# Optimization experiments

Measured on AMD Instinct MI355X. Metric: run time of the kernel, lower is better.

Reference implementation:

```python
import jax, jax.numpy as jnp
import numpy as np

# ---- constant lookup tables (mirror SoftALU registered buffers) ----
def _build_tables():
    n = np.arange(16)
    A, Bq, C = np.meshgrid(n, n, np.arange(2), indexing='ij')
    total = A + Bq + C
    eye16 = np.eye(16, dtype=np.float32)
    eye2 = np.eye(2, dtype=np.float32)
    add_t = eye16[total % 16]        # (16,16,2,16)
    carry_t = eye2[total // 16]      # (16,16,2,2)
    and_t = eye16[n[:, None] & n[None, :]]
    or_t = eye16[n[:, None] | n[None, :]]
    xor_t = eye16[n[:, None] ^ n[None, :]]
    bb = np.arange(256)
    b2n = np.zeros((256, 32), np.float32)
    b2n[bb, bb >> 4] = 1.0
    b2n[bb, 16 + (bb & 15)] = 1.0
    return tuple(jnp.asarray(t) for t in (add_t, carry_t, and_t, or_t, xor_t, b2n, b2n.T))

ADD_T, CARRY_T, AND_T, OR_T, XOR_T, B2N, N2B = _build_tables()
_SHIFTS = jnp.arange(4, dtype=jnp.uint32) * jnp.uint32(8)
SHARP = 100.0  # softmax sharpening temperature from the original module


def _sharp(x):
    return jax.nn.softmax(SHARP * x, axis=-1)


def _to_nibbles(x):  # x: (B,4,256) -> (high, low) each (B,4,16)
    comb = jnp.einsum('bnc,cm->bnm', x, B2N)
    return _sharp(comb[..., :16]), _sharp(comb[..., 16:])


def _from_nibbles(high, low):  # (...,16),(...,16) -> (...,256)
    return _sharp(jnp.einsum('...m,mc->...c', jnp.concatenate([high, low], axis=-1), N2B))


def _nibble_add(a, b, cin):  # (B,16),(B,16),(B,2) -> sum (B,16), carry (B,2)
    w = jnp.einsum('bi,bj,bk->bijk', a, b, cin)
    s = jnp.einsum('bijk,ijkl->bl', w, ADD_T)
    c = jnp.einsum('bijk,ijkl->bl', w, CARRY_T)
    return _sharp(s), _sharp(c)


def soft_add(a, b):  # (B,4,256) x2 -> (B,4,256), little-endian ripple-carry over 8 nibbles
    ah, al = _to_nibbles(a)
    bh, bl = _to_nibbles(b)
    carry = jnp.broadcast_to(jnp.array([1.0, 0.0], dtype=a.dtype), (a.shape[0], 2))
    out = []
    for i in range(4):  # fixed 4-byte carry recurrence (structural, not data dim)
        s_lo, carry = _nibble_add(al[:, i], bl[:, i], carry)
        s_hi, carry = _nibble_add(ah[:, i], bh[:, i], carry)
        out.append(_from_nibbles(s_hi, s_lo))
    return jnp.stack(out, axis=1)


def soft_bitwise(a, b, table):
    ah, al = _to_nibbles(a)
    bh, bl = _to_nibbles(b)
    r_hi = _sharp(jnp.einsum('bni,bnj,ijk->bnk', ah, bh, table))
    r_lo = _sharp(jnp.einsum('bni,bnj,ijk->bnk', al, bl, table))
    return _from_nibbles(r_hi, r_lo)


def _encode_u32(v):  # (B,) uint32 -> (B,4,256) one-hot bytes (little-endian)
    bytes_ = (v[:, None] >> _SHIFTS) & jnp.uint32(255)
    return jax.nn.one_hot(bytes_, 256, dtype=jnp.float32)


def _decode_u32(x):  # (B,4,256) -> (B,) uint32 (argmax decode, as in module.decode)
    bytes_ = jnp.argmax(x, axis=-1).astype(jnp.uint32)
    return (bytes_ << _SHIFTS).sum(axis=-1).astype(jnp.uint32)


def soft_negate(x):  # two's complement: xor with 0xFF per byte, then +1
    xh, xl = _to_nibbles(x)
    xf = XOR_T[:, 15, :]  # xor-with-0xF map (0xF is an exact one-hot in the original)
    f_hi = _sharp(jnp.einsum('bni,ik->bnk', xh, xf))
    f_lo = _sharp(jnp.einsum('bni,ik->bnk', xl, xf))
    flipped = _from_nibbles(f_hi, f_lo)
    one = _encode_u32(jnp.ones((x.shape[0],), dtype=jnp.uint32))
    return soft_add(flipped, one)


def soft_mul(a, b):
    # Original: decode -> silu(a)*b + silu(-a)*(-b) == exact a*b -> round -> encode.
    # Exact integer product mod 2^32 (encode masks to 32 bits).
    return _encode_u32(_decode_u32(a) * _decode_u32(b))


def soft_div(a, b):
    # decode() yields unsigned 0..2^32-1, so the original's repeated-subtraction
    # loop computes unsigned integer division, with b==0 -> 0.
    av, bv = _decode_u32(a), _decode_u32(b)
    q = jnp.where(bv == jnp.uint32(0), jnp.uint32(0), av // jnp.maximum(bv, jnp.uint32(1)))
    return _encode_u32(q)


def setup_inputs() -> dict:
    key = jax.random.key(0)
    k1, k2 = jax.random.split(key)
    Bsz = 8192
    a = jax.nn.one_hot(jax.random.randint(k1, (Bsz, 4), 0, 256), 256, dtype=jnp.float32)
    b = jax.nn.one_hot(jax.random.randint(k2, (Bsz, 4), 0, 256), 256, dtype=jnp.float32)
    return {"a": a, "b": b}


def reference(a, b):
    # all_ops(): (add, sub, mul, div, and, or, xor) each (B,4,256) -> (7,B,4,256)
    return jnp.stack([
        soft_add(a, b),
        soft_add(a, soft_negate(b)),  # subtract = a + (~b + 1)
        soft_mul(a, b),
        soft_div(a, b),
        soft_bitwise(a, b, AND_T),
        soft_bitwise(a, b, OR_T),
        soft_bitwise(a, b, XOR_T),
    ], axis=0)
```

## Files before the change

### kernel.cpp

```cpp
#include <hip/hip_runtime.h>
#include <stdint.h>


__global__ __launch_bounds__(256) void softalu_kernel(const float* __restrict__ a,
                                                      const float* __restrict__ b,
                                                      float* __restrict__ out,
                                                      int B) {
    const int batch = blockIdx.x;
    const int t = threadIdx.x;

    __shared__ uint32_t sh_bytes[8];
    __shared__ uint32_t res[7];

    const float* pa = a + (size_t)batch * 1024;
    const float* pb = b + (size_t)batch * 1024;
#pragma unroll
    for (int n = 0; n < 4; ++n) {
        if (pa[n * 256 + t] > 0.5f) sh_bytes[n] = (uint32_t)t;
        if (pb[n * 256 + t] > 0.5f) sh_bytes[4 + n] = (uint32_t)t;
    }
    __syncthreads();

    if (t == 0) {
        const uint32_t av = sh_bytes[0] | (sh_bytes[1] << 8) | (sh_bytes[2] << 16) | (sh_bytes[3] << 24);
        const uint32_t bv = sh_bytes[4] | (sh_bytes[5] << 8) | (sh_bytes[6] << 16) | (sh_bytes[7] << 24);
        res[0] = av + bv;
        res[1] = av - bv;
        res[2] = av * bv;
        res[3] = bv ? (av / bv) : 0u;
        res[4] = av & bv;
        res[5] = av | bv;
        res[6] = av ^ bv;
    }
    __syncthreads();

    const int n = t >> 6;
    const int lane4 = t & 63;
    const int c0 = lane4 * 4;

#pragma unroll
    for (int op = 0; op < 7; ++op) {
        const int rb = (int)((res[op] >> (8 * n)) & 255u);
        float4 v;
        v.x = (c0 + 0 == rb) ? 1.0f : 0.0f;
        v.y = (c0 + 1 == rb) ? 1.0f : 0.0f;
        v.z = (c0 + 2 == rb) ? 1.0f : 0.0f;
        v.w = (c0 + 3 == rb) ? 1.0f : 0.0f;
        float4* dst = (float4*)(out + (((size_t)op * B + batch) * 4 + n) * 256) + lane4;
        *dst = v;
    }
}

extern "C" void kernel_launch(void* const* d_in, const int* in_sizes, int n_in,
                              void* d_out, int out_size, void* d_ws, size_t ws_size,
                              hipStream_t stream) {
    const float* a = (const float*)d_in[0];
    const float* b = (const float*)d_in[1];
    float* out = (float*)d_out;
    const int B = in_sizes[0] / (4 * 256);
    softalu_kernel<<<B, 256, 0, stream>>>(a, b, out, B);
}
```

Before: 290.7 us.

## Split into decode and streaming writer kernels with nontemporal stores

Splits the single kernel in two. The first decodes the input bytes and writes the seven 32-bit results per batch into workspace. The second is a grid-stride writer that expands those results into one-hot float4 rows, writing them contiguously with nontemporal stores. This aims to make the large output write stream better and avoid the per-block syncs and serial thread-0 compute in the writer phase. In exchange it adds a second launch and a small workspace round trip.

```diff
diff --git a/kernel.cpp b/kernel.cpp
--- a/kernel.cpp
+++ b/kernel.cpp
@@ -2,15 +2,16 @@
 #include <stdint.h>
 
 
-__global__ __launch_bounds__(256) void softalu_kernel(const float* __restrict__ a,
-                                                      const float* __restrict__ b,
-                                                      float* __restrict__ out,
-                                                      int B) {
+typedef float vfloat4 __attribute__((ext_vector_type(4)));
+
+__global__ __launch_bounds__(256) void decode_kernel(const float* __restrict__ a,
+                                                     const float* __restrict__ b,
+                                                     uint32_t* __restrict__ res,
+                                                     int B) {
     const int batch = blockIdx.x;
     const int t = threadIdx.x;
 
     __shared__ uint32_t sh_bytes[8];
-    __shared__ uint32_t res[7];
 
     const float* pa = a + (size_t)batch * 1024;
     const float* pb = b + (size_t)batch * 1024;
@@ -24,30 +25,35 @@
     if (t == 0) {
         const uint32_t av = sh_bytes[0] | (sh_bytes[1] << 8) | (sh_bytes[2] << 16) | (sh_bytes[3] << 24);
         const uint32_t bv = sh_bytes[4] | (sh_bytes[5] << 8) | (sh_bytes[6] << 16) | (sh_bytes[7] << 24);
-        res[0] = av + bv;
-        res[1] = av - bv;
-        res[2] = av * bv;
-        res[3] = bv ? (av / bv) : 0u;
-        res[4] = av & bv;
-        res[5] = av | bv;
-        res[6] = av ^ bv;
+        res[0 * B + batch] = av + bv;
+        res[1 * B + batch] = av - bv;
+        res[2 * B + batch] = av * bv;
+        res[3 * B + batch] = bv ? (av / bv) : 0u;
+        res[4 * B + batch] = av & bv;
+        res[5 * B + batch] = av | bv;
+        res[6 * B + batch] = av ^ bv;
     }
-    __syncthreads();
+}
 
-    const int n = t >> 6;
-    const int lane4 = t & 63;
-    const int c0 = lane4 * 4;
-
-#pragma unroll
-    for (int op = 0; op < 7; ++op) {
-        const int rb = (int)((res[op] >> (8 * n)) & 255u);
-        float4 v;
+__global__ __launch_bounds__(256) void writer_kernel(const uint32_t* __restrict__ res,
+                                                     vfloat4* __restrict__ out,
+                                                     int B) {
+    const size_t total = (size_t)7 * B * 4 * 64;
+    const size_t stride = (size_t)gridDim.x * blockDim.x;
+    for (size_t g = (size_t)blockIdx.x * blockDim.x + threadIdx.x; g < total; g += stride) {
+        const int lane4 = (int)(g & 63);
+        const size_t row = g >> 6;
+        const int n = (int)(row & 3);
+        const int ob = __builtin_amdgcn_readfirstlane((int)(row >> 2));
+        const uint32_t r = res[ob];
+        const int rb = (int)((r >> (8 * n)) & 255u);
+        const int c0 = lane4 * 4;
+        vfloat4 v;
         v.x = (c0 + 0 == rb) ? 1.0f : 0.0f;
         v.y = (c0 + 1 == rb) ? 1.0f : 0.0f;
         v.z = (c0 + 2 == rb) ? 1.0f : 0.0f;
         v.w = (c0 + 3 == rb) ? 1.0f : 0.0f;
-        float4* dst = (float4*)(out + (((size_t)op * B + batch) * 4 + n) * 256) + lane4;
-        *dst = v;
+        __builtin_nontemporal_store(v, &out[g]);
     }
 }
 
@@ -58,5 +64,8 @@
     const float* b = (const float*)d_in[1];
     float* out = (float*)d_out;
     const int B = in_sizes[0] / (4 * 256);
-    softalu_kernel<<<B, 256, 0, stream>>>(a, b, out, B);
+    uint32_t* res = (uint32_t*)d_ws;
+
+    decode_kernel<<<B, 256, 0, stream>>>(a, b, res, B);
+    writer_kernel<<<4096, 256, 0, stream>>>(res, (vfloat4*)out, B);
 }
```

Result: no change. 286.9 us (-1.3%).

## Zero output with memset and scatter one-hot ones instead of dense writes

Applied to the files above, without the earlier changes.

Replaces the per-block dense one-hot write of all 7x4x256 floats with a hipMemsetAsync that zeroes the whole output, followed by a kernel that writes only the single 1.0 per output row. Input loads are vectorised to float4 per thread, and the single-thread compute plus second barrier is replaced by 28 threads each computing one op/byte. The output is still written in full by the memset, which may be faster than kernel stores, but it adds a second launch and scattered single-float stores.

```diff
diff --git a/kernel.cpp b/kernel.cpp
--- a/kernel.cpp
+++ b/kernel.cpp
@@ -2,52 +2,47 @@
 #include <stdint.h>
 
 
-__global__ __launch_bounds__(256) void softalu_kernel(const float* __restrict__ a,
-                                                      const float* __restrict__ b,
-                                                      float* __restrict__ out,
-                                                      int B) {
+typedef float vfloat4 __attribute__((ext_vector_type(4)));
+
+__global__ __launch_bounds__(256) void decode_scatter_kernel(const float* __restrict__ a,
+                                                             const float* __restrict__ b,
+                                                             float* __restrict__ out,
+                                                             int B) {
     const int batch = blockIdx.x;
     const int t = threadIdx.x;
 
     __shared__ uint32_t sh_bytes[8];
-    __shared__ uint32_t res[7];
 
-    const float* pa = a + (size_t)batch * 1024;
-    const float* pb = b + (size_t)batch * 1024;
+    const vfloat4* va = (const vfloat4*)(a + (size_t)batch * 1024);
+    const vfloat4* vb = (const vfloat4*)(b + (size_t)batch * 1024);
+    const vfloat4 xa = va[t];
+    const vfloat4 xb = vb[t];
+    const int row = t >> 6;
+    const int pos0 = (t & 63) * 4;
 #pragma unroll
-    for (int n = 0; n < 4; ++n) {
-        if (pa[n * 256 + t] > 0.5f) sh_bytes[n] = (uint32_t)t;
-        if (pb[n * 256 + t] > 0.5f) sh_bytes[4 + n] = (uint32_t)t;
+    for (int j = 0; j < 4; ++j) {
+        if (xa[j] > 0.5f) sh_bytes[row] = (uint32_t)(pos0 + j);
+        if (xb[j] > 0.5f) sh_bytes[4 + row] = (uint32_t)(pos0 + j);
     }
     __syncthreads();
 
-    if (t == 0) {
-        const uint32_t av = sh_bytes[0] | (sh_bytes[1] << 8) | (sh_bytes[2] << 16) | (sh_bytes[3] << 24);
-        const uint32_t bv = sh_bytes[4] | (sh_bytes[5] << 8) | (sh_bytes[6] << 16) | (sh_bytes[7] << 24);
-        res[0] = av + bv;
-        res[1] = av - bv;
-        res[2] = av * bv;
-        res[3] = bv ? (av / bv) : 0u;
-        res[4] = av & bv;
-        res[5] = av | bv;
-        res[6] = av ^ bv;
-    }
-    __syncthreads();
-
-    const int n = t >> 6;
-    const int lane4 = t & 63;
-    const int c0 = lane4 * 4;
-
-#pragma unroll
-    for (int op = 0; op < 7; ++op) {
-        const int rb = (int)((res[op] >> (8 * n)) & 255u);
-        float4 v;
-        v.x = (c0 + 0 == rb) ? 1.0f : 0.0f;
-        v.y = (c0 + 1 == rb) ? 1.0f : 0.0f;
-        v.z = (c0 + 2 == rb) ? 1.0f : 0.0f;
-        v.w = (c0 + 3 == rb) ? 1.0f : 0.0f;
-        float4* dst = (float4*)(out + (((size_t)op * B + batch) * 4 + n) * 256) + lane4;
-        *dst = v;
+    const uint32_t av = sh_bytes[0] | (sh_bytes[1] << 8) | (sh_bytes[2] << 16) | (sh_bytes[3] << 24);
+    const uint32_t bv = sh_bytes[4] | (sh_bytes[5] << 8) | (sh_bytes[6] << 16) | (sh_bytes[7] << 24);
+    if (t < 28) {
+        const int op = t >> 2;
+        const int n  = t & 3;
+        uint32_t r;
+        switch (op) {
+            case 0: r = av + bv; break;
+            case 1: r = av - bv; break;
+            case 2: r = av * bv; break;
+            case 3: r = bv ? (av / bv) : 0u; break;
+            case 4: r = av & bv; break;
+            case 5: r = av | bv; break;
+            default: r = av ^ bv; break;
+        }
+        const int rb = (int)((r >> (8 * n)) & 255u);
+        out[(((size_t)op * B + batch) * 4 + n) * 256 + rb] = 1.0f;
     }
 }
 
@@ -58,5 +53,7 @@
     const float* b = (const float*)d_in[1];
     float* out = (float*)d_out;
     const int B = in_sizes[0] / (4 * 256);
-    softalu_kernel<<<B, 256, 0, stream>>>(a, b, out, B);
+
+    hipMemsetAsync(out, 0, (size_t)out_size * sizeof(float), stream);
+    decode_scatter_kernel<<<B, 256, 0, stream>>>(a, b, out, B);
 }
```

Measured after the change: 289.5 us. Within noise of the previous version (-0.4%).
